# Kernel optimization log

Measured on AMD Instinct MI355X. Metric: run time of the kernel, lower is better.

## Reference

```python
import jax, jax.numpy as jnp
import numpy as np

C = 64          # channels
K = 15          # sum(shell_sizes)=1+14
H = 32          # neighbors per query
N = 50000       # support points (== query points M)
RADIUS = 1.0
SIGMA = 0.7
INF = 1e6
BN_EPS = 1e-5


def _init_kernel_points(key):
    # stand-in for load_kernels: 1 center point + 14 points on a sphere shell
    pts = jax.random.normal(key, (K - 1, 3), dtype=jnp.float32)
    pts = pts / jnp.linalg.norm(pts, axis=1, keepdims=True) * RADIUS
    return jnp.concatenate([jnp.zeros((1, 3), jnp.float32), pts], axis=0)


def setup_inputs() -> dict:
    key = jax.random.key(0)
    ks = jax.random.split(key, 10)
    q_pts = jax.random.normal(ks[0], (N, 3), dtype=jnp.float32)
    s_pts = jax.random.normal(ks[1], (N, 3), dtype=jnp.float32)
    s_feats = jax.random.normal(ks[2], (N, C), dtype=jnp.float32)
    neighb_inds = jax.random.randint(ks[3], (N, H), 0, N)
    kernel_points = _init_kernel_points(ks[4])
    # alpha_mlp: Linear(C->C, no bias) -> BatchNorm -> LeakyReLU(0.1) -> Linear(C->K*C)
    lim1 = 1.0 / np.sqrt(C)
    W1 = jax.random.uniform(ks[5], (C, C), jnp.float32, -lim1, lim1)
    gamma = jnp.ones((C,), jnp.float32)
    beta = jnp.zeros((C,), jnp.float32)
    W2 = jax.random.uniform(ks[6], (C, K * C), jnp.float32, -lim1, lim1)
    b2 = jax.random.uniform(ks[7], (K * C,), jnp.float32, -lim1, lim1)
    return {"q_pts": q_pts, "s_pts": s_pts, "s_feats": s_feats,
            "neighb_inds": neighb_inds, "kernel_points": kernel_points,
            "W1": W1, "gamma": gamma, "beta": beta, "W2": W2, "b2": b2}


def reference(q_pts, s_pts, s_feats, neighb_inds, kernel_points, W1, gamma, beta, W2, b2):
    M = q_pts.shape[0]
    # alpha_mlp on pooled (= center) features: (M, C) -> (M, K*C)
    h = s_feats @ W1
    mu = jnp.mean(h, axis=0)
    var = jnp.var(h, axis=0)
    h = (h - mu) / jnp.sqrt(var + BN_EPS) * gamma + beta
    h = jax.nn.leaky_relu(h, 0.1)
    conv_weights = (h @ W2 + b2).reshape(M, K, C)

    # gather neighbor features with a zero padding row (index N -> zeros)
    padded_feats = jnp.concatenate([s_feats, jnp.zeros((1, C), s_feats.dtype)], axis=0)
    neighbor_feats = padded_feats[neighb_inds]                 # (M, H, C)

    # relative neighbor positions with inf padding point
    s_pts_pad = jnp.concatenate([s_pts, jnp.full((1, 3), INF, s_pts.dtype)], axis=0)
    neighbors = s_pts_pad[neighb_inds] - q_pts[:, None, :]     # (M, H, 3)

    # kernel-point influence: nearest kernel point + linear influence
    diff = neighbors[:, :, None, :] - kernel_points            # (M, H, K, 3)
    sq_d = jnp.sum(diff * diff, axis=-1)                       # (M, H, K)
    nn_sq = jnp.min(sq_d, axis=-1)                             # (M, H)
    nn_idx = jnp.argmin(sq_d, axis=-1)                         # (M, H)
    infl = jnp.clip(1.0 - jnp.sqrt(nn_sq) / SIGMA, 0.0)        # (M, H)

    # per-neighbor channel weights from the MLP output, gathered by 1nn kernel point
    nw = jnp.take_along_axis(conv_weights, nn_idx[:, :, None], axis=1)  # (M, H, C)
    nw = nw * infl[:, :, None]

    # weighted aggregation (merge=mul, aggr=sum over neighbors)
    return jnp.sum(neighbor_feats * nw, axis=1)                # (M, C)
```

## Files before the change

### kernel.cpp

```cpp
#include <hip/hip_runtime.h>
#include <hip/hip_bf16.h>
#include <math.h>

#define N_PTS 50000
#define CCH   64
#define KP    15
#define NH    32
#define SIGMA 0.7f
#define BN_EPS 1e-5f
#define LEAKY 0.1f
#define QB    16
#define CWS   18
#define STATS_BLOCKS 1024

typedef short bf16x8 __attribute__((ext_vector_type(8)));
typedef float floatx4 __attribute__((ext_vector_type(4)));

__device__ __forceinline__ unsigned short f2b(float f) {
    union { float f; unsigned u; } v; v.f = f;
    return (unsigned short)((v.u + 0x7FFFu + ((v.u >> 16) & 1u)) >> 16);
}
__device__ __forceinline__ ushort2 f2b2(float a, float b) {
    __hip_bfloat162 h = __float22bfloat162_rn(float2{a, b});
    union { __hip_bfloat162 h; ushort2 u; } v; v.h = h;
    return v.u;
}
__device__ __forceinline__ float b2f(unsigned short b) {
    union { unsigned u; float f; } v; v.u = ((unsigned)b) << 16;
    return v.f;
}

__global__ __launch_bounds__(256) void k_prep(const float* __restrict__ sf,
                                              const float* __restrict__ W1,
                                              const float* __restrict__ W2,
                                              float* __restrict__ bn,
                                              unsigned short* __restrict__ hst,
                                              unsigned short* __restrict__ w2b,
                                              unsigned short* __restrict__ sfb) {
    int t = threadIdx.x;
    if (blockIdx.x >= STATS_BLOCKS) {
        int g = (blockIdx.x - STATS_BLOCKS) * 256 + t;
        int lane = g & 63, s = (g >> 6) & 1, tt = g >> 7;
        int col = lane & 15, quad = lane >> 4;
        int base = (s * 32 + quad * 8) * 960 + tt * 16 + col;
        ushort4 lo, hi;
        lo.x = f2b(W2[base + 0 * 960]); lo.y = f2b(W2[base + 1 * 960]);
        lo.z = f2b(W2[base + 2 * 960]); lo.w = f2b(W2[base + 3 * 960]);
        hi.x = f2b(W2[base + 4 * 960]); hi.y = f2b(W2[base + 5 * 960]);
        hi.z = f2b(W2[base + 6 * 960]); hi.w = f2b(W2[base + 7 * 960]);
        *(ushort4*)(w2b + g * 8)     = lo;
        *(ushort4*)(w2b + g * 8 + 4) = hi;
        return;
    }
    int c = t & 63, ml = t >> 6;
    float w1c[64];
    #pragma unroll
    for (int i = 0; i < 64; ++i) w1c[i] = W1[i * 64 + c];
    __shared__ float rows[4][64];
    float acc_s = 0.f, acc_q = 0.f;
    for (int m0 = blockIdx.x * 4; m0 < N_PTS; m0 += STATS_BLOCKS * 4) {
        __syncthreads();
        float v = sf[m0 * 64 + t];
        ((float*)rows)[t] = v;
        sfb[m0 * 64 + t] = f2b(v);
        __syncthreads();
        float h = 0.f;
        #pragma unroll
        for (int i4 = 0; i4 < 16; ++i4) {
            float4 r = *(const float4*)&rows[ml][i4 * 4];
            h += r.x * w1c[i4 * 4] + r.y * w1c[i4 * 4 + 1]
               + r.z * w1c[i4 * 4 + 2] + r.w * w1c[i4 * 4 + 3];
        }
        acc_s += h;
        acc_q += h * h;
        hst[(m0 + ml) * 64 + c] = f2b(h);
    }
    __shared__ float red[2][256];
    red[0][t] = acc_s; red[1][t] = acc_q;
    __syncthreads();
    if (t < 64) {
        float s = red[0][t] + red[0][64 + t] + red[0][128 + t] + red[0][192 + t];
        float q = red[1][t] + red[1][64 + t] + red[1][128 + t] + red[1][192 + t];
        atomicAdd(&bn[t], s);
        atomicAdd(&bn[64 + t], q);
    }
}

__global__ __launch_bounds__(256, 4) void k_main(
    const float* __restrict__ q_pts, const float* __restrict__ s_pts,
    const unsigned short* __restrict__ sfb, const int* __restrict__ nb,
    const float* __restrict__ kpts, const float* __restrict__ gamma,
    const float* __restrict__ beta, const float* __restrict__ bn,
    const float* __restrict__ b2, const unsigned short* __restrict__ w2b,
    const unsigned short* __restrict__ hst, float* __restrict__ out) {

    __shared__ __align__(16) unsigned short cwT[960 * CWS];
    __shared__ float abS[128];
    __shared__ int      nCnt[QB];
    __shared__ __align__(16) unsigned nPack[QB][NH];
    __shared__ __align__(16) float    nInf[QB][NH];

    int t = threadIdx.x;
    int lane = t & 63, wv = t >> 6;
    int m0 = blockIdx.x * QB;

    if (t < 64) {
        float mu  = bn[t] * (1.0f / N_PTS);
        float var = bn[64 + t] * (1.0f / N_PTS) - mu * mu;
        float a   = gamma[t] * rsqrtf(var + BN_EPS);
        abS[t]      = a;
        abS[64 + t] = beta[t] - mu * a;
    } else if (t >= 64 && t < 64 + QB) {
        nCnt[t - 64] = 0;
    }
    ((unsigned*)nPack)[t]    = 0u;
    ((unsigned*)nPack)[t + 256] = 0u;
    ((float*)nInf)[t]        = 0.f;
    ((float*)nInf)[t + 256]  = 0.f;
    __syncthreads();

    int row = lane & 15, half = lane >> 4;
    bf16x8 a0, a1;
    {
        const unsigned short* hrow = hst + (m0 + row) * 64 + half * 8;
        bf16x8 r0 = *(const bf16x8*)(hrow);
        bf16x8 r1 = *(const bf16x8*)(hrow + 32);
        #pragma unroll
        for (int j = 0; j < 8; j += 2) {
            int c0 = half * 8 + j;
            float g0 = abS[c0] * b2f((unsigned short)r0[j]) + abS[64 + c0];
            float g1 = abS[c0 + 1] * b2f((unsigned short)r0[j + 1]) + abS[64 + c0 + 1];
            g0 = g0 > 0.f ? g0 : LEAKY * g0;
            g1 = g1 > 0.f ? g1 : LEAKY * g1;
            ushort2 p01 = f2b2(g0, g1);
            a0[j] = (short)p01.x; a0[j + 1] = (short)p01.y;
            int c1 = 32 + c0;
            float g2 = abS[c1] * b2f((unsigned short)r1[j]) + abS[64 + c1];
            float g3 = abS[c1 + 1] * b2f((unsigned short)r1[j + 1]) + abS[64 + c1 + 1];
            g2 = g2 > 0.f ? g2 : LEAKY * g2;
            g3 = g3 > 0.f ? g3 : LEAKY * g3;
            ushort2 p23 = f2b2(g2, g3);
            a1[j] = (short)p23.x; a1[j + 1] = (short)p23.y;
        }
    }

    {
        int col = lane & 15, quad = lane >> 4;
        for (int ti = 0; ti < 15; ++ti) {
            int tt = wv * 15 + ti;
            bf16x8 bf0 = *(const bf16x8*)(w2b + ((tt * 2 + 0) * 64 + lane) * 8);
            bf16x8 bf1 = *(const bf16x8*)(w2b + ((tt * 2 + 1) * 64 + lane) * 8);
            floatx4 acc = {0.f, 0.f, 0.f, 0.f};
            acc = __builtin_amdgcn_mfma_f32_16x16x32_bf16(a0, bf0, acc, 0, 0, 0);
            acc = __builtin_amdgcn_mfma_f32_16x16x32_bf16(a1, bf1, acc, 0, 0, 0);
            int n = tt * 16 + col;
            float bb = b2[n];
            unsigned short* dst = &cwT[n * CWS + quad * 4];
            ushort2 w01 = f2b2(acc[0] + bb, acc[1] + bb);
            ushort2 w23 = f2b2(acc[2] + bb, acc[3] + bb);
            *(ushort2*)(dst)     = w01;
            *(ushort2*)(dst + 2) = w23;
        }
    }

    float kpr[45];
    #pragma unroll
    for (int i = 0; i < 45; ++i) kpr[i] = kpts[i];

    for (int task = t; task < QB * NH; task += 256) {
        int q = task >> 5, hh = task & 31;
        int m = m0 + q;
        int idx = nb[m * NH + hh];
        float px = s_pts[idx * 3 + 0] - q_pts[m * 3 + 0];
        float py = s_pts[idx * 3 + 1] - q_pts[m * 3 + 1];
        float pz = s_pts[idx * 3 + 2] - q_pts[m * 3 + 2];
        float best = 1e30f; int bi = 0;
        #pragma unroll
        for (int k = 0; k < KP; ++k) {
            float dx = px - kpr[k * 3], dy = py - kpr[k * 3 + 1], dz = pz - kpr[k * 3 + 2];
            float d = dx * dx + dy * dy + dz * dz;
            if (d < best) { best = d; bi = k; }
        }
        float infl = 1.f - sqrtf(best) * (1.0f / SIGMA);
        if (infl > 0.f) {
            int pos = atomicAdd(&nCnt[q], 1);
            nPack[q][pos] = (unsigned)idx | ((unsigned)(bi * (64 * CWS)) << 16);
            nInf[q][pos]  = infl;
        }
    }
    __syncthreads();

    {
        int c = lane;
        #pragma unroll
        for (int pp = 0; pp < 2; ++pp) {
            int qa = wv * 4 + pp * 2, qb = qa + 1;
            const unsigned short* cwa = cwT + c * CWS + qa;
            const unsigned short* cwb = cwa + 1;
            int nA = nCnt[qa], nB = nCnt[qb];
            int na = nA > nB ? nA : nB;
            float accA = 0.f, accB = 0.f;
            for (int jj = 0; jj < na; jj += 4) {
                uint4  pa = *(const uint4*)&nPack[qa][jj];
                uint4  pb = *(const uint4*)&nPack[qb][jj];
                float4 ia = *(const float4*)&nInf[qa][jj];
                float4 ib = *(const float4*)&nInf[qb][jj];
                float fA0 = b2f(sfb[(pa.x & 0xFFFFu) * 64 + c]);
                float fA1 = b2f(sfb[(pa.y & 0xFFFFu) * 64 + c]);
                float fA2 = b2f(sfb[(pa.z & 0xFFFFu) * 64 + c]);
                float fA3 = b2f(sfb[(pa.w & 0xFFFFu) * 64 + c]);
                float fB0 = b2f(sfb[(pb.x & 0xFFFFu) * 64 + c]);
                float fB1 = b2f(sfb[(pb.y & 0xFFFFu) * 64 + c]);
                float fB2 = b2f(sfb[(pb.z & 0xFFFFu) * 64 + c]);
                float fB3 = b2f(sfb[(pb.w & 0xFFFFu) * 64 + c]);
                float wA0 = b2f(cwa[pa.x >> 16]);
                float wA1 = b2f(cwa[pa.y >> 16]);
                float wA2 = b2f(cwa[pa.z >> 16]);
                float wA3 = b2f(cwa[pa.w >> 16]);
                float wB0 = b2f(cwb[pb.x >> 16]);
                float wB1 = b2f(cwb[pb.y >> 16]);
                float wB2 = b2f(cwb[pb.z >> 16]);
                float wB3 = b2f(cwb[pb.w >> 16]);
                accA += ia.x * fA0 * wA0 + ia.y * fA1 * wA1
                      + ia.z * fA2 * wA2 + ia.w * fA3 * wA3;
                accB += ib.x * fB0 * wB0 + ib.y * fB1 * wB1
                      + ib.z * fB2 * wB2 + ib.w * fB3 * wB3;
            }
            out[(m0 + qa) * 64 + c] = accA;
            out[(m0 + qb) * 64 + c] = accB;
        }
    }
}

extern "C" void kernel_launch(void* const* d_in, const int* in_sizes, int n_in,
                              void* d_out, int out_size, void* d_ws, size_t ws_size,
                              hipStream_t stream) {
    const float* q_pts   = (const float*)d_in[0];
    const float* s_pts   = (const float*)d_in[1];
    const float* s_feats = (const float*)d_in[2];
    const int*   nb      = (const int*)d_in[3];
    const float* kpts    = (const float*)d_in[4];
    const float* W1      = (const float*)d_in[5];
    const float* gamma   = (const float*)d_in[6];
    const float* beta    = (const float*)d_in[7];
    const float* W2      = (const float*)d_in[8];
    const float* b2      = (const float*)d_in[9];
    float* out = (float*)d_out;

    float* ws = (float*)d_ws;
    float* bn = ws;
    unsigned short* w2b = (unsigned short*)(ws + 128);
    unsigned short* hst = w2b + 61440;
    unsigned short* sfb = hst + N_PTS * CCH;

    hipMemsetAsync(bn, 0, 128 * sizeof(float), stream);
    k_prep<<<STATS_BLOCKS + 30, 256, 0, stream>>>(s_feats, W1, W2, bn, hst, w2b, sfb);
    k_main<<<N_PTS / QB, 256, 0, stream>>>(q_pts, s_pts, sfb, nb, kpts,
                                           gamma, beta, bn, b2, w2b, hst, out);
}
```

Measured before the change: 161.3 us.

## Move neighbor kernel-point classification into prep kernel with packed global list

The per-neighbor nearest-kernel-point search and influence computation move out of k_main into extra blocks of k_prep. Those blocks write a compacted, zero-padded neighbor list to global memory, packing index, kernel id and a 12-bit quantized influence into one word per neighbor. k_main then reads these packed lists and drops its shared-memory staging and one phase of its work. The aim is to overlap the classification with the stats/GEMM prep and shorten k_main. The cost is an extra global round-trip for the packed list and reduced influence precision from quantization.

```diff
diff --git a/kernel.cpp b/kernel.cpp
--- a/kernel.cpp
+++ b/kernel.cpp
@@ -12,6 +12,9 @@
 #define QB    16
 #define CWS   18
 #define STATS_BLOCKS 1024
+#define W2P_BLOCKS   30
+#define QC           64
+#define CLS_BLOCKS   782
 
 typedef short bf16x8 __attribute__((ext_vector_type(8)));
 typedef float floatx4 __attribute__((ext_vector_type(4)));
@@ -33,11 +36,58 @@
 __global__ __launch_bounds__(256) void k_prep(const float* __restrict__ sf,
                                               const float* __restrict__ W1,
                                               const float* __restrict__ W2,
+                                              const float* __restrict__ q_pts,
+                                              const float* __restrict__ s_pts,
+                                              const int* __restrict__ nb,
+                                              const float* __restrict__ kpts,
                                               float* __restrict__ bn,
                                               unsigned short* __restrict__ hst,
                                               unsigned short* __restrict__ w2b,
-                                              unsigned short* __restrict__ sfb) {
+                                              unsigned short* __restrict__ sfb,
+                                              unsigned* __restrict__ packG,
+                                              int* __restrict__ cntG) {
     int t = threadIdx.x;
+    if (blockIdx.x >= STATS_BLOCKS + W2P_BLOCKS) {
+        int q0 = (blockIdx.x - (STATS_BLOCKS + W2P_BLOCKS)) * QC;
+        __shared__ int cnt[QC];
+        for (int i = t; i < QC; i += 256) cnt[i] = 0;
+        float kpr[45];
+        #pragma unroll
+        for (int i = 0; i < 45; ++i) kpr[i] = kpts[i];
+        __syncthreads();
+        for (int task = t; task < QC * NH; task += 256) {
+            int ql = task >> 5, hh = task & 31;
+            int m = q0 + ql;
+            if (m >= N_PTS) continue;
+            int idx = nb[m * NH + hh];
+            float px = s_pts[idx * 3 + 0] - q_pts[m * 3 + 0];
+            float py = s_pts[idx * 3 + 1] - q_pts[m * 3 + 1];
+            float pz = s_pts[idx * 3 + 2] - q_pts[m * 3 + 2];
+            float best = 1e30f; int bi = 0;
+            #pragma unroll
+            for (int k = 0; k < KP; ++k) {
+                float dx = px - kpr[k*3], dy = py - kpr[k*3+1], dz = pz - kpr[k*3+2];
+                float d = dx * dx + dy * dy + dz * dz;
+                if (d < best) { best = d; bi = k; }
+            }
+            float infl = 1.f - sqrtf(best) * (1.0f / SIGMA);
+            if (infl > 0.f) {
+                int iq = (int)(infl * 4095.f + 0.5f);
+                int pos = atomicAdd(&cnt[ql], 1);
+                packG[m * NH + pos] = (unsigned)idx | ((unsigned)bi << 16)
+                                    | ((unsigned)iq << 20);
+            }
+        }
+        __syncthreads();
+        for (int i = t; i < QC * NH; i += 256) {
+            int ql = i >> 5, j = i & 31;
+            int m = q0 + ql;
+            if (m >= N_PTS) continue;
+            if (j >= cnt[ql]) packG[m * NH + j] = 0u;
+            if (j == 0) cntG[m] = cnt[ql];
+        }
+        return;
+    }
     if (blockIdx.x >= STATS_BLOCKS) {
         int g = (blockIdx.x - STATS_BLOCKS) * 256 + t;
         int lane = g & 63, s = (g >> 6) & 1, tt = g >> 7;
@@ -87,18 +137,15 @@
 }
 
 __global__ __launch_bounds__(256, 4) void k_main(
-    const float* __restrict__ q_pts, const float* __restrict__ s_pts,
-    const unsigned short* __restrict__ sfb, const int* __restrict__ nb,
-    const float* __restrict__ kpts, const float* __restrict__ gamma,
-    const float* __restrict__ beta, const float* __restrict__ bn,
-    const float* __restrict__ b2, const unsigned short* __restrict__ w2b,
-    const unsigned short* __restrict__ hst, float* __restrict__ out) {
+    const unsigned short* __restrict__ sfb,
+    const float* __restrict__ gamma, const float* __restrict__ beta,
+    const float* __restrict__ bn, const float* __restrict__ b2,
+    const unsigned short* __restrict__ w2b, const unsigned short* __restrict__ hst,
+    const unsigned* __restrict__ packG, const int* __restrict__ cntG,
+    float* __restrict__ out) {
 
     __shared__ __align__(16) unsigned short cwT[960 * CWS];
     __shared__ float abS[128];
-    __shared__ int      nCnt[QB];
-    __shared__ __align__(16) unsigned nPack[QB][NH];
-    __shared__ __align__(16) float    nInf[QB][NH];
 
     int t = threadIdx.x;
     int lane = t & 63, wv = t >> 6;
@@ -110,13 +157,7 @@
         float a   = gamma[t] * rsqrtf(var + BN_EPS);
         abS[t]      = a;
         abS[64 + t] = beta[t] - mu * a;
-    } else if (t >= 64 && t < 64 + QB) {
-        nCnt[t - 64] = 0;
-    }
-    ((unsigned*)nPack)[t]    = 0u;
-    ((unsigned*)nPack)[t + 256] = 0u;
-    ((float*)nInf)[t]        = 0.f;
-    ((float*)nInf)[t + 256]  = 0.f;
+    }
     __syncthreads();
 
     int row = lane & 15, half = lane >> 4;
@@ -162,72 +203,54 @@
             *(ushort2*)(dst + 2) = w23;
         }
     }
-
-    float kpr[45];
-    #pragma unroll
-    for (int i = 0; i < 45; ++i) kpr[i] = kpts[i];
-
-    for (int task = t; task < QB * NH; task += 256) {
-        int q = task >> 5, hh = task & 31;
-        int m = m0 + q;
-        int idx = nb[m * NH + hh];
-        float px = s_pts[idx * 3 + 0] - q_pts[m * 3 + 0];
-        float py = s_pts[idx * 3 + 1] - q_pts[m * 3 + 1];
-        float pz = s_pts[idx * 3 + 2] - q_pts[m * 3 + 2];
-        float best = 1e30f; int bi = 0;
-        #pragma unroll
-        for (int k = 0; k < KP; ++k) {
-            float dx = px - kpr[k * 3], dy = py - kpr[k * 3 + 1], dz = pz - kpr[k * 3 + 2];
-            float d = dx * dx + dy * dy + dz * dz;
-            if (d < best) { best = d; bi = k; }
-        }
-        float infl = 1.f - sqrtf(best) * (1.0f / SIGMA);
-        if (infl > 0.f) {
-            int pos = atomicAdd(&nCnt[q], 1);
-            nPack[q][pos] = (unsigned)idx | ((unsigned)(bi * (64 * CWS)) << 16);
-            nInf[q][pos]  = infl;
-        }
-    }
     __syncthreads();
 
     {
+        int wvu = __builtin_amdgcn_readfirstlane(wv);
         int c = lane;
         #pragma unroll
         for (int pp = 0; pp < 2; ++pp) {
-            int qa = wv * 4 + pp * 2, qb = qa + 1;
+            int qa = wvu * 4 + pp * 2, qb = qa + 1;
+            int ma = m0 + qa, mb = m0 + qb;
+            const unsigned* pA = packG + ma * NH;
+            const unsigned* pB = packG + mb * NH;
             const unsigned short* cwa = cwT + c * CWS + qa;
             const unsigned short* cwb = cwa + 1;
-            int nA = nCnt[qa], nB = nCnt[qb];
-            int na = nA > nB ? nA : nB;
+            int cA = cntG[ma], cB = cntG[mb];
+            int na = cA > cB ? cA : cB;
+            na = (na + 3) & ~3;
             float accA = 0.f, accB = 0.f;
             for (int jj = 0; jj < na; jj += 4) {
-                uint4  pa = *(const uint4*)&nPack[qa][jj];
-                uint4  pb = *(const uint4*)&nPack[qb][jj];
-                float4 ia = *(const float4*)&nInf[qa][jj];
-                float4 ib = *(const float4*)&nInf[qb][jj];
-                float fA0 = b2f(sfb[(pa.x & 0xFFFFu) * 64 + c]);
-                float fA1 = b2f(sfb[(pa.y & 0xFFFFu) * 64 + c]);
-                float fA2 = b2f(sfb[(pa.z & 0xFFFFu) * 64 + c]);
-                float fA3 = b2f(sfb[(pa.w & 0xFFFFu) * 64 + c]);
-                float fB0 = b2f(sfb[(pb.x & 0xFFFFu) * 64 + c]);
-                float fB1 = b2f(sfb[(pb.y & 0xFFFFu) * 64 + c]);
-                float fB2 = b2f(sfb[(pb.z & 0xFFFFu) * 64 + c]);
-                float fB3 = b2f(sfb[(pb.w & 0xFFFFu) * 64 + c]);
-                float wA0 = b2f(cwa[pa.x >> 16]);
-                float wA1 = b2f(cwa[pa.y >> 16]);
-                float wA2 = b2f(cwa[pa.z >> 16]);
-                float wA3 = b2f(cwa[pa.w >> 16]);
-                float wB0 = b2f(cwb[pb.x >> 16]);
-                float wB1 = b2f(cwb[pb.y >> 16]);
-                float wB2 = b2f(cwb[pb.z >> 16]);
-                float wB3 = b2f(cwb[pb.w >> 16]);
-                accA += ia.x * fA0 * wA0 + ia.y * fA1 * wA1
-                      + ia.z * fA2 * wA2 + ia.w * fA3 * wA3;
-                accB += ib.x * fB0 * wB0 + ib.y * fB1 * wB1
-                      + ib.z * fB2 * wB2 + ib.w * fB3 * wB3;
+                unsigned pa0 = pA[jj], pa1 = pA[jj+1], pa2 = pA[jj+2], pa3 = pA[jj+3];
+                unsigned pb0 = pB[jj], pb1 = pB[jj+1], pb2 = pB[jj+2], pb3 = pB[jj+3];
+                float fA0 = b2f(sfb[(pa0 & 0xFFFFu) * 64 + c]);
+                float fA1 = b2f(sfb[(pa1 & 0xFFFFu) * 64 + c]);
+                float fA2 = b2f(sfb[(pa2 & 0xFFFFu) * 64 + c]);
+                float fA3 = b2f(sfb[(pa3 & 0xFFFFu) * 64 + c]);
+                float fB0 = b2f(sfb[(pb0 & 0xFFFFu) * 64 + c]);
+                float fB1 = b2f(sfb[(pb1 & 0xFFFFu) * 64 + c]);
+                float fB2 = b2f(sfb[(pb2 & 0xFFFFu) * 64 + c]);
+                float fB3 = b2f(sfb[(pb3 & 0xFFFFu) * 64 + c]);
+                float wA0 = b2f(cwa[((pa0 >> 16) & 15u) * (64 * CWS)]);
+                float wA1 = b2f(cwa[((pa1 >> 16) & 15u) * (64 * CWS)]);
+                float wA2 = b2f(cwa[((pa2 >> 16) & 15u) * (64 * CWS)]);
+                float wA3 = b2f(cwa[((pa3 >> 16) & 15u) * (64 * CWS)]);
+                float wB0 = b2f(cwb[((pb0 >> 16) & 15u) * (64 * CWS)]);
+                float wB1 = b2f(cwb[((pb1 >> 16) & 15u) * (64 * CWS)]);
+                float wB2 = b2f(cwb[((pb2 >> 16) & 15u) * (64 * CWS)]);
+                float wB3 = b2f(cwb[((pb3 >> 16) & 15u) * (64 * CWS)]);
+                float iA0 = (float)(pa0 >> 20), iA1 = (float)(pa1 >> 20);
+                float iA2 = (float)(pa2 >> 20), iA3 = (float)(pa3 >> 20);
+                float iB0 = (float)(pb0 >> 20), iB1 = (float)(pb1 >> 20);
+                float iB2 = (float)(pb2 >> 20), iB3 = (float)(pb3 >> 20);
+                accA += iA0 * fA0 * wA0 + iA1 * fA1 * wA1
+                      + iA2 * fA2 * wA2 + iA3 * fA3 * wA3;
+                accB += iB0 * fB0 * wB0 + iB1 * fB1 * wB1
+                      + iB2 * fB2 * wB2 + iB3 * fB3 * wB3;
             }
-            out[(m0 + qa) * 64 + c] = accA;
-            out[(m0 + qb) * 64 + c] = accB;
+            const float qs = 1.f / 4095.f;
+            out[ma * 64 + c] = accA * qs;
+            out[mb * 64 + c] = accB * qs;
         }
     }
 }
@@ -252,9 +275,12 @@
     unsigned short* w2b = (unsigned short*)(ws + 128);
     unsigned short* hst = w2b + 61440;
     unsigned short* sfb = hst + N_PTS * CCH;
+    unsigned* packG = (unsigned*)(sfb + N_PTS * CCH);
+    int* cntG = (int*)(packG + N_PTS * NH);
 
     hipMemsetAsync(bn, 0, 128 * sizeof(float), stream);
-    k_prep<<<STATS_BLOCKS + 30, 256, 0, stream>>>(s_feats, W1, W2, bn, hst, w2b, sfb);
-    k_main<<<N_PTS / QB, 256, 0, stream>>>(q_pts, s_pts, sfb, nb, kpts,
-                                           gamma, beta, bn, b2, w2b, hst, out);
-}
+    k_prep<<<STATS_BLOCKS + W2P_BLOCKS + CLS_BLOCKS, 256, 0, stream>>>(
+        s_feats, W1, W2, q_pts, s_pts, nb, kpts, bn, hst, w2b, sfb, packG, cntG);
+    k_main<<<N_PTS / QB, 256, 0, stream>>>(sfb, gamma, beta, bn, b2, w2b, hst,
+                                           packG, cntG, out);
+}
```

New measurement: 162.3 us. Within noise of the previous version (+0.6%).
